# Kernel optimization log

Hardware: AMD Instinct MI355X
Metric: run time of the kernel (lower is better)

Reference implementation:

```python
import jax, jax.numpy as jnp
import numpy as np

C = 64; H = 80; W = 120; B = 2; V = 3; BV = B * V; D = 20
NEAR = 0.1; FAR = 100.0
BF16 = jnp.bfloat16


def conv2d(x, w, b, pad):
    y = jax.lax.conv_general_dilated(x, w, (1, 1), [(pad, pad), (pad, pad)],
                                     dimension_numbers=('NCHW', 'OIHW', 'NCHW'))
    return y + b[None, :, None, None]


def bn2d(x, g, b, m, v, eps=1e-5):
    # BatchNorm2d in inference mode (running stats)
    scale = g / jnp.sqrt(v + eps)
    return (x - m[None, :, None, None]) * scale[None, :, None, None] + b[None, :, None, None]


def grid_sample(feat, grid):
    # feat [N,C,Hf,Wf], grid [N,Hg,Wg,2] in [-1,1]; bilinear, zeros padding, align_corners=True
    _, _, Hf, Wf = feat.shape
    gx = (grid[..., 0] + 1.0) * 0.5 * (Wf - 1)
    gy = (grid[..., 1] + 1.0) * 0.5 * (Hf - 1)
    x0 = jnp.floor(gx); y0 = jnp.floor(gy)

    def one(f, gx, gy, x0, y0):
        def gather(xi, yi):
            valid = (xi >= 0) & (xi < Wf) & (yi >= 0) & (yi < Hf)
            xc = jnp.clip(xi, 0, Wf - 1).astype(jnp.int32)
            yc = jnp.clip(yi, 0, Hf - 1).astype(jnp.int32)
            return f[:, yc, xc] * valid.astype(f.dtype)
        wx = gx - x0; wy = gy - y0
        return (gather(x0, y0) * ((1 - wx) * (1 - wy))
                + gather(x0 + 1, y0) * (wx * (1 - wy))
                + gather(x0, y0 + 1) * ((1 - wx) * wy)
                + gather(x0 + 1, y0 + 1) * (wx * wy))
    return jax.vmap(one)(feat, gx, gy, x0, y0)


def forward(x, intrinsics, c2ws,
            pf_bn1_g, pf_bn1_b, pf_bn1_m, pf_bn1_v, pf_w1, pf_b1,
            pf_bn2_g, pf_bn2_b, pf_bn2_m, pf_bn2_v, pf_w2, pf_b2,
            cp_w, cp_b, cf_bn_g, cf_bn_b, cf_bn_m, cf_bn_v, cf_w, cf_b):
    # ---- flag[0]: predicted depth -> world xyz, position_fusion ----
    depth = 255.0 * (0.5 * jnp.tanh(x[:, 0]) + 0.5)                       # [BV,H,W]
    d16 = depth.astype(BF16)
    ug = jnp.broadcast_to(jnp.arange(W, dtype=jnp.float32)[None, :], (H, W)).astype(BF16)
    vg = jnp.broadcast_to(jnp.arange(H, dtype=jnp.float32)[:, None], (H, W)).astype(BF16)
    cam = jnp.stack([ug[None] * d16, vg[None] * d16, d16], axis=-1).reshape(BV, H * W, 3)
    Kinv = jnp.linalg.inv(intrinsics.astype(jnp.float32)).astype(BF16)
    xyz = jnp.einsum('nij,npj->npi', Kinv, cam)                           # cam coords
    xyz = jnp.einsum('nij,npj->npi', c2ws[:, :3, :3].astype(BF16), xyz) \
          + c2ws[:, :3, 3].astype(BF16)[:, None, :]                       # world coords
    xyz = xyz.reshape(BV, H, W, 3).transpose(0, 3, 1, 2).astype(x.dtype)
    h = jnp.concatenate([xyz, x], axis=1)                                 # [BV,C+3,H,W]
    h = jax.nn.silu(conv2d(bn2d(h, pf_bn1_g, pf_bn1_b, pf_bn1_m, pf_bn1_v), pf_w1, pf_b1, 4))
    h = jax.nn.silu(conv2d(bn2d(h, pf_bn2_g, pf_bn2_b, pf_bn2_m, pf_bn2_v), pf_w2, pf_b2, 4))

    # ---- flag[1]: multi-view plane-sweep correlation ----
    xr = h.reshape(B, V, C, H, W)
    vb = lambda t: t.transpose(1, 0, 2, 3, 4).reshape(BV, C, H, W)        # 'b v ... -> (v b) ...'
    feat01 = vb(xr)
    Ki = intrinsics.reshape(B, V, 3, 3)
    intr_curr = jax.lax.stop_gradient(
        (Ki * jnp.array([W, H, 1.0], jnp.float32)[None, None, :, None]).transpose(1, 0, 2, 3).reshape(BV, 3, 3))
    E = jax.lax.stop_gradient(c2ws.reshape(B, V, 4, 4))
    Einv = jnp.linalg.inv(E)
    dmin, dmax = 1.0 / FAR, 1.0 / NEAR
    depth_vals = 1.0 / (dmin + jnp.linspace(0.0, 1.0, D) * (dmax - dmin))  # [D]
    pix = jnp.stack([jnp.broadcast_to(jnp.arange(W, dtype=jnp.float32)[None, :], (H, W)),
                     jnp.broadcast_to(jnp.arange(H, dtype=jnp.float32)[:, None], (H, W)),
                     jnp.ones((H, W), jnp.float32)], 0).reshape(3, H * W)
    Kinv_c = jnp.linalg.inv(intr_curr).astype(BF16)

    corr = 0.0
    for idx in range(1, V):
        order = list(range(V))[idx:] + list(range(V))[:idx]
        feat10 = vb(xr[:, jnp.array(order)])                              # [BV,C,H,W]
        pose = jnp.concatenate([E[:, o] @ Einv[:, v0] for v0, o in enumerate(order)], axis=0)  # [BV,4,4]
        pts = jnp.einsum('bij,jp->bip', Kinv_c, pix.astype(BF16))
        pts = jnp.einsum('bij,bjp->bip', pose[:, :3, :3].astype(BF16), pts)
        pts = pts[:, :, None, :] * depth_vals.astype(BF16)[None, None, :, None] \
              + pose[:, :3, 3].astype(BF16)[:, :, None, None]             # [BV,3,D,HW]
        pts = jnp.einsum('bij,bjdp->bidp', intr_curr.astype(BF16), pts).astype(jnp.float32)
        den = jnp.maximum(pts[:, 2], 1e-3)
        grid = jnp.stack([2.0 * pts[:, 0] / den / (W - 1) - 1.0,
                          2.0 * pts[:, 1] / den / (H - 1) - 1.0], axis=-1)
        grid = jax.lax.stop_gradient(grid.reshape(BV, D * H, W, 2))
        warped = grid_sample(feat10, grid).reshape(BV, C, D, H, W)
        corr = corr + jnp.einsum('bchw,bcdhw->bdhw', feat01, warped) / (C ** 0.5)
    corr = corr / (V - 1)

    cin = jnp.concatenate([corr, feat01], axis=1)                         # [BV,D+C,H,W]
    cost = conv2d(cin, cp_w, cp_b, 1).reshape(V, B, C, H, W).transpose(1, 0, 2, 3, 4)
    fused = jnp.concatenate([cost, xr], axis=2).reshape(BV, 2 * C, H, W)
    out = jax.nn.silu(conv2d(bn2d(fused, cf_bn_g, cf_bn_b, cf_bn_m, cf_bn_v), cf_w, cf_b, 4))
    return out


def setup_inputs() -> dict:
    key = jax.random.key(0)
    ks = jax.random.split(key, 24)
    def nrm(i, shape, scale=1.0):
        return scale * jax.random.normal(ks[i], shape, jnp.float32)
    def wconv(i, shape):
        fan_in = int(np.prod(shape[1:]))
        return jax.random.normal(ks[i], shape, jnp.float32) / np.sqrt(fan_in)
    x = nrm(0, (BV, C, H, W))
    Kmat = np.tile(np.array([[1.2, 0, 0.5], [0, 1.6, 0.5], [0, 0, 1.0]], np.float32), (BV, 1, 1))
    intrinsics = jnp.asarray(Kmat)
    c2_list = []
    for i in range(BV):
        th = 0.3 * (i % V) - 0.3
        T = np.eye(4, dtype=np.float32)
        T[:3, :3] = np.array([[np.cos(th), 0, np.sin(th)], [0, 1, 0], [-np.sin(th), 0, np.cos(th)]], np.float32)
        T[:3, 3] = [0.5 * (i % V) - 0.5, 0.0, 0.1]
        c2_list.append(T)
    c2ws = jnp.asarray(np.stack(c2_list))
    # first BN sees raw world-xyz channels (magnitude ~1e4), so realistic running var there
    bn1_v = jnp.concatenate([jnp.full((3,), 1e8, jnp.float32), jnp.ones((C,), jnp.float32)])
    return dict(
        x=x, intrinsics=intrinsics, c2ws=c2ws,
        pf_bn1_g=1.0 + 0.1 * nrm(1, (C + 3,)), pf_bn1_b=0.1 * nrm(2, (C + 3,)),
        pf_bn1_m=0.1 * nrm(3, (C + 3,)), pf_bn1_v=bn1_v,
        pf_w1=wconv(4, (C, C + 3, 9, 9)), pf_b1=0.01 * nrm(5, (C,)),
        pf_bn2_g=1.0 + 0.1 * nrm(6, (C,)), pf_bn2_b=0.1 * nrm(7, (C,)),
        pf_bn2_m=0.1 * nrm(8, (C,)), pf_bn2_v=jnp.ones((C,), jnp.float32),
        pf_w2=wconv(9, (C, C, 9, 9)), pf_b2=0.01 * nrm(10, (C,)),
        cp_w=wconv(11, (C, C + D, 3, 3)), cp_b=0.01 * nrm(12, (C,)),
        cf_bn_g=1.0 + 0.1 * nrm(13, (2 * C,)), cf_bn_b=0.1 * nrm(14, (2 * C,)),
        cf_bn_m=0.1 * nrm(15, (2 * C,)), cf_bn_v=jnp.ones((2 * C,), jnp.float32),
        cf_w=wconv(16, (C, 2 * C, 9, 9)), cf_b=0.01 * nrm(17, (C,)))


def reference(x, intrinsics, c2ws,
              pf_bn1_g, pf_bn1_b, pf_bn1_m, pf_bn1_v, pf_w1, pf_b1,
              pf_bn2_g, pf_bn2_b, pf_bn2_m, pf_bn2_v, pf_w2, pf_b2,
              cp_w, cp_b, cf_bn_g, cf_bn_b, cf_bn_m, cf_bn_v, cf_w, cf_b):
    return forward(x, intrinsics, c2ws,
                   pf_bn1_g, pf_bn1_b, pf_bn1_m, pf_bn1_v, pf_w1, pf_b1,
                   pf_bn2_g, pf_bn2_b, pf_bn2_m, pf_bn2_v, pf_w2, pf_b2,
                   cp_w, cp_b, cf_bn_g, cf_bn_b, cf_bn_m, cf_bn_v, cf_w, cf_b)
```

## Files before the change

kernel.cpp:

```cpp
#include <hip/hip_runtime.h>
#include <math.h>

static constexpr int kH  = 80;
static constexpr int kW  = 120;
static constexpr int kHW = kH * kW;
static constexpr int kBV = 6;
static constexpr int kD  = 20;

typedef __attribute__((ext_vector_type(8)))  short bf16x8;
typedef __attribute__((ext_vector_type(16))) float f32x16;
typedef __attribute__((ext_vector_type(4)))  int   i32x4;
typedef __attribute__((ext_vector_type(2)))  int   i32x2;
typedef __attribute__((ext_vector_type(4)))  float float4v;

__device__ __forceinline__ float bf16r(float x) {
  unsigned u = __float_as_uint(x);
  u += 0x7FFFu + ((u >> 16) & 1u);
  return __uint_as_float(u & 0xFFFF0000u);
}
__device__ __forceinline__ unsigned short bf16c(float x) {
  unsigned u = __float_as_uint(x);
  u += 0x7FFFu + ((u >> 16) & 1u);
  return (unsigned short)(u >> 16);
}
__device__ __forceinline__ int pack2(float a, float b) {
  return (int)((unsigned)bf16c(a) | ((unsigned)bf16c(b) << 16));
}
__device__ __forceinline__ float bl(unsigned pk) {
  return __uint_as_float(pk << 16);
}
__device__ __forceinline__ float bh(unsigned pk) {
  return __uint_as_float(pk & 0xFFFF0000u);
}

struct ConstBuf {
  float bn1_s[67], bn1_o[67];
  float bn2_s[64], bn2_o[64];
  float bnf_s[128], bnf_o[128];
  float Kinv[6][9];
  float Rw[6][9];
  float tw[6][3];
  float Kinvc[6][9];
  float intrc[6][9];
  float poseR[2][6][9];
  float poseT[2][6][3];
  float dvals[20];
};

__device__ void inv3x3(const float* A, float* o) {
  float a = A[0], b = A[1], c = A[2];
  float d = A[3], e = A[4], f = A[5];
  float g = A[6], h = A[7], i = A[8];
  float det = a * (e * i - f * h) - b * (d * i - f * g) + c * (d * h - e * g);
  float id = 1.0f / det;
  o[0] = (e * i - f * h) * id;
  o[1] = -(b * i - c * h) * id;
  o[2] = (b * f - c * e) * id;
  o[3] = -(d * i - f * g) * id;
  o[4] = (a * i - c * g) * id;
  o[5] = -(a * f - c * d) * id;
  o[6] = (d * h - e * g) * id;
  o[7] = -(a * h - b * g) * id;
  o[8] = (a * e - b * d) * id;
}

__device__ void inv4x4(const float* A, float* out) {
  float M[4][8];
  for (int r = 0; r < 4; ++r) {
    for (int c = 0; c < 4; ++c) M[r][c] = A[r * 4 + c];
    for (int c = 0; c < 4; ++c) M[r][4 + c] = (r == c) ? 1.0f : 0.0f;
  }
  for (int col = 0; col < 4; ++col) {
    int p = col;
    float best = fabsf(M[col][col]);
    for (int r = col + 1; r < 4; ++r) {
      float v = fabsf(M[r][col]);
      if (v > best) { best = v; p = r; }
    }
    if (p != col)
      for (int c = 0; c < 8; ++c) { float t = M[col][c]; M[col][c] = M[p][c]; M[p][c] = t; }
    float inv = 1.0f / M[col][col];
    for (int c = 0; c < 8; ++c) M[col][c] *= inv;
    for (int r = 0; r < 4; ++r) {
      if (r == col) continue;
      float f = M[r][col];
      for (int c = 0; c < 8; ++c) M[r][c] -= f * M[col][c];
    }
  }
  for (int r = 0; r < 4; ++r)
    for (int c = 0; c < 4; ++c) out[r * 4 + c] = M[r][4 + c];
}

__device__ void mm4(const float* A, const float* B, float* C) {
  for (int r = 0; r < 4; ++r)
    for (int c = 0; c < 4; ++c) {
      float s = 0.0f;
      for (int k = 0; k < 4; ++k) s += A[r * 4 + k] * B[k * 4 + c];
      C[r * 4 + c] = s;
    }
}

__global__ void consts_kernel(const float* __restrict__ intr, const float* __restrict__ c2,
                              const float* g1, const float* b1, const float* m1, const float* v1,
                              const float* g2, const float* b2, const float* m2, const float* v2,
                              const float* gf, const float* bff, const float* mf, const float* vff,
                              ConstBuf* cb) {
  int tid = threadIdx.x;
  for (int c = tid; c < 67; c += 64) {
    float s = g1[c] / sqrtf(v1[c] + 1e-5f);
    cb->bn1_s[c] = s; cb->bn1_o[c] = b1[c] - m1[c] * s;
  }
  for (int c = tid; c < 64; c += 64) {
    float s = g2[c] / sqrtf(v2[c] + 1e-5f);
    cb->bn2_s[c] = s; cb->bn2_o[c] = b2[c] - m2[c] * s;
  }
  for (int c = tid; c < 128; c += 64) {
    float s = gf[c] / sqrtf(vff[c] + 1e-5f);
    cb->bnf_s[c] = s; cb->bnf_o[c] = bff[c] - mf[c] * s;
  }
  if (tid < 20) {
    float l = (1.0f / 19.0f) * (float)tid;
    cb->dvals[tid] = bf16r(1.0f / (0.01f + l * 9.99f));
  }
  __shared__ float Einv_s[6][16];
  if (tid < 6) {
    float Ki[9];
    inv3x3(intr + tid * 9, Ki);
    for (int k = 0; k < 9; ++k) cb->Kinv[tid][k] = bf16r(Ki[k]);
    const float* T = c2 + tid * 16;
    cb->Rw[tid][0] = bf16r(T[0]);  cb->Rw[tid][1] = bf16r(T[1]);  cb->Rw[tid][2] = bf16r(T[2]);
    cb->Rw[tid][3] = bf16r(T[4]);  cb->Rw[tid][4] = bf16r(T[5]);  cb->Rw[tid][5] = bf16r(T[6]);
    cb->Rw[tid][6] = bf16r(T[8]);  cb->Rw[tid][7] = bf16r(T[9]);  cb->Rw[tid][8] = bf16r(T[10]);
    cb->tw[tid][0] = bf16r(T[3]);  cb->tw[tid][1] = bf16r(T[7]);  cb->tw[tid][2] = bf16r(T[11]);
    inv4x4(T, Einv_s[tid]);
    int vj = tid >> 1, bj = tid & 1, ii = bj * 3 + vj;
    const float* Kk = intr + ii * 9;
    float S[9] = {Kk[0] * 120.0f, Kk[1] * 120.0f, Kk[2] * 120.0f,
                  Kk[3] * 80.0f,  Kk[4] * 80.0f,  Kk[5] * 80.0f,
                  Kk[6],          Kk[7],          Kk[8]};
    for (int k = 0; k < 9; ++k) cb->intrc[tid][k] = bf16r(S[k]);
    float Si[9];
    inv3x3(S, Si);
    for (int k = 0; k < 9; ++k) cb->Kinvc[tid][k] = bf16r(Si[k]);
  }
  __syncthreads();
  if (tid < 12) {
    int t = tid / 6, jj = tid % 6;
    int vj = jj >> 1, bj = jj & 1;
    int o = (vj + t + 1) % 3;
    float P[16];
    mm4(c2 + (bj * 3 + o) * 16, Einv_s[bj * 3 + vj], P);
    for (int r = 0; r < 3; ++r) {
      for (int c = 0; c < 3; ++c) cb->poseR[t][jj][r * 3 + c] = bf16r(P[r * 4 + c]);
      cb->poseT[t][jj][r] = bf16r(P[r * 4 + 3]);
    }
  }
}

template <int K, int CINP, int CINR>
__global__ __launch_bounds__(256)
void prep_w(const float* __restrict__ w, unsigned short* __restrict__ Wp) {
  constexpr int NCH = CINP / 32;
  constexpr int NU = K * K * NCH * 256;
  int u = blockIdx.x * 256 + threadIdx.x;
  if (u >= NU) return;
  int slot = u & 255;
  int rest = u >> 8;
  int ci = rest % NCH;
  int kk = rest / NCH;
  int ky = kk / K, kx = kk - ky * K;
  int q = slot >> 6, lu = slot & 63;
  int nt = q >> 1, kc = q & 1;
  int oc = nt * 32 + (lu & 31);
  int gi = kc * 2 + (lu >> 5);
  int chb = ci * 32 + gi * 8;
  unsigned short o[8];
#pragma unroll
  for (int e = 0; e < 8; ++e) {
    int ch = chb + e;
    float val = (ch < CINR) ? w[(((size_t)oc * CINR + ch) * K + ky) * K + kx] : 0.0f;
    o[e] = bf16c(val);
  }
  i32x4 pk;
  pk.x = (int)o[0] | ((int)o[1] << 16);
  pk.y = (int)o[2] | ((int)o[3] << 16);
  pk.z = (int)o[4] | ((int)o[5] << 16);
  pk.w = (int)o[6] | ((int)o[7] << 16);
  *(i32x4*)&Wp[(size_t)u * 8] = pk;
}

__global__ __launch_bounds__(256)
void hn_pack(const float* __restrict__ x, const ConstBuf* __restrict__ cb,
             unsigned short* __restrict__ hn_b) {
  int id = blockIdx.x * 256 + threadIdx.x;
  if (id >= kBV * kHW) return;
  int bv = id / kHW, pix = id - bv * kHW;
  int yy = pix / kW, xx = pix - yy * kW;
  float t0 = tanhf(x[(size_t)bv * 64 * kHW + pix]);
  float depth = 255.0f * (0.5f * t0 + 0.5f);
  float dz = bf16r(depth);
  float cx = bf16r((float)xx * dz);
  float cy = bf16r((float)yy * dz);
  const float* Ki = cb->Kinv[bv];
  float p0 = bf16r(Ki[0] * cx + Ki[1] * cy + Ki[2] * dz);
  float p1 = bf16r(Ki[3] * cx + Ki[4] * cy + Ki[5] * dz);
  float p2 = bf16r(Ki[6] * cx + Ki[7] * cy + Ki[8] * dz);
  const float* R = cb->Rw[bv];
  const float* tw = cb->tw[bv];
  float q[3];
  q[0] = bf16r(bf16r(R[0] * p0 + R[1] * p1 + R[2] * p2) + tw[0]);
  q[1] = bf16r(bf16r(R[3] * p0 + R[4] * p1 + R[5] * p2) + tw[1]);
  q[2] = bf16r(bf16r(R[6] * p0 + R[7] * p1 + R[8] * p2) + tw[2]);
  unsigned short* o = &hn_b[(size_t)id * 96];
  const float* xb = x + (size_t)bv * 64 * kHW + pix;
#pragma unroll
  for (int g = 0; g < 24; ++g) {
    float vv[4];
#pragma unroll
    for (int e = 0; e < 4; ++e) {
      int ch = g * 4 + e;
      float val;
      if (ch < 3) val = q[ch] * cb->bn1_s[ch] + cb->bn1_o[ch];
      else if (ch < 67) val = xb[(size_t)(ch - 3) * kHW] * cb->bn1_s[ch] + cb->bn1_o[ch];
      else val = 0.0f;
      vv[e] = val;
    }
    i32x2 pk = {pack2(vv[0], vv[1]), pack2(vv[2], vv[3])};
    *(i32x2*)(o + g * 4) = pk;
  }
}

template <int CINP, int K, int OUT>
__global__ __launch_bounds__(256)
void conv_mfma(const unsigned short* __restrict__ in_b,
               const unsigned short* __restrict__ Wp,
               const float* __restrict__ bias,
               const ConstBuf* __restrict__ cb,
               float* __restrict__ outf,
               unsigned short* __restrict__ outb,
               unsigned short* __restrict__ outb2) {
  constexpr int NCH = CINP / 32;
  constexpr int KK = K * K;
  constexpr int KH0 = (KK + 1) / 2;
  constexpr int PAD = K / 2;
  constexpr int NC = 16 + K - 1;
  constexpr int NR = 8 + K - 1;
  constexpr int NPX = NC * NR;
  __shared__ unsigned short sA[NPX * 32];

  const int tid = threadIdx.x;
  const int w = tid >> 6, l = tid & 63;
  const int half = w >> 1, mp = w & 1;
  const int bx = blockIdx.x, by = blockIdx.y, bz = blockIdx.z;
  const size_t inbase = (size_t)bz * kHW;

  const int r = l & 31, h = l >> 5;
  const int xloc = r & 15, rhi = r >> 4;
  const int kk0 = half ? KH0 : 0;
  const int myKK = half ? (KK - KH0) : KH0;
  f32x16 acc[2][2] = {};

  for (int ci = 0; ci < NCH; ++ci) {
    __syncthreads();
    for (int g2 = tid; g2 < NPX * 4; g2 += 256) {
      int px = g2 >> 2, gi = g2 & 3;
      int hy = px / NC, hx = px - hy * NC;
      int gy = by * 8 - PAD + hy, gx = bx * 16 - PAD + hx;
      bool ok = ((unsigned)gy < (unsigned)kH) && ((unsigned)gx < (unsigned)kW);
      i32x4 v = {0, 0, 0, 0};
      if (ok) v = *(const i32x4*)&in_b[(inbase + gy * kW + gx) * CINP + ci * 32 + gi * 8];
      *(i32x4*)&sA[px * 32 + ((gi ^ ((px >> 2) & 3)) << 3)] = v;
    }
    __syncthreads();

    const unsigned short* wb = Wp + ((size_t)ci * 256 + (size_t)kk0 * NCH * 256) * 8;
    const size_t kstep = (size_t)NCH * 256 * 8;
#define LOADB(dst, rdidx)                                                       \
    {                                                                           \
      const unsigned short* bp = wb + (size_t)(rdidx) * kstep + (size_t)l * 8;  \
      dst[0][0] = *(const bf16x8*)(bp);                                         \
      dst[0][1] = *(const bf16x8*)(bp + 64 * 8);                                \
      dst[1][0] = *(const bf16x8*)(bp + 128 * 8);                               \
      dst[1][1] = *(const bf16x8*)(bp + 192 * 8);                               \
    }
#define COMPUTE(rdidx, bb)                                                      \
    {                                                                           \
      const int kk = kk0 + (rdidx);                                             \
      const int ky = kk / K, kx = kk - ky * K;                                  \
      bf16x8 a[2][2];                                                           \
      _Pragma("unroll")                                                         \
      for (int m = 0; m < 2; ++m) {                                             \
        const int hp = (4 * mp + 2 * m + rhi + ky) * NC + (xloc + kx);          \
        _Pragma("unroll")                                                       \
        for (int kc = 0; kc < 2; ++kc) {                                        \
          int gi = kc * 2 + h;                                                  \
          a[m][kc] = *(const bf16x8*)&sA[hp * 32 + ((gi ^ ((hp >> 2) & 3)) << 3)]; \
        }                                                                       \
      }                                                                         \
      _Pragma("unroll")                                                         \
      for (int m = 0; m < 2; ++m)                                               \
        _Pragma("unroll")                                                       \
        for (int nt = 0; nt < 2; ++nt) {                                        \
          acc[m][nt] = __builtin_amdgcn_mfma_f32_32x32x16_bf16(a[m][0], bb[nt][0], acc[m][nt], 0, 0, 0); \
          acc[m][nt] = __builtin_amdgcn_mfma_f32_32x32x16_bf16(a[m][1], bb[nt][1], acc[m][nt], 0, 0, 0); \
        }                                                                       \
    }

    bf16x8 b0[2][2], b1[2][2];
    LOADB(b0, 0);
    int rd = 0;
    for (; rd + 2 <= myKK; rd += 2) {
      LOADB(b1, rd + 1);
      COMPUTE(rd, b0);
      if (rd + 2 < myKK) LOADB(b0, rd + 2);
      COMPUTE(rd + 1, b1);
    }
    if (rd < myKK) COMPUTE(rd, b0);
#undef LOADB
#undef COMPUTE
  }

  float* scratch = (float*)sA;
#pragma unroll
  for (int cm = 0; cm < 2; ++cm) {
#pragma unroll
    for (int cn = 0; cn < 2; ++cn) {
      float* sp = scratch + ((mp * 64 + l) * 16);
      __syncthreads();
      if (half == 1) {
#pragma unroll
        for (int q = 0; q < 16; ++q) sp[q] = acc[cm][cn][q];
      }
      __syncthreads();
      if (half == 0) {
#pragma unroll
        for (int q = 0; q < 16; ++q) acc[cm][cn][q] += sp[q];
      }
    }
  }
  if (half == 1) return;

#pragma unroll
  for (int m = 0; m < 2; ++m) {
#pragma unroll
    for (int nt = 0; nt < 2; ++nt) {
      const int oc = nt * 32 + (l & 31);
      const float bs = bias[oc];
      float s2 = 0.f, o2 = 0.f;
      if (OUT == 0) { s2 = cb->bn2_s[oc]; o2 = cb->bn2_o[oc]; }
      if (OUT == 1) { s2 = cb->bnf_s[64 + oc]; o2 = cb->bnf_o[64 + oc]; }
      if (OUT == 2) { s2 = cb->bnf_s[oc]; o2 = cb->bnf_o[oc]; }
#pragma unroll
      for (int reg = 0; reg < 16; ++reg) {
        int row = (reg & 3) + 8 * (reg >> 2) + 4 * h;
        int x = bx * 16 + (row & 15);
        if (x >= kW) continue;
        int y = by * 8 + 4 * mp + 2 * m + (row >> 4);
        float v = acc[m][nt][reg] + bs;
        if (OUT != 2) v = v / (1.0f + expf(-v));
        if (OUT == 0) {
          size_t px = inbase + y * kW + x;
          outb[px * 64 + oc] = bf16c(v * s2 + o2);
        } else if (OUT == 1) {
          size_t px = inbase + y * kW + x;
          outb[px * 64 + oc] = bf16c(v);
          outb2[px * 128 + 64 + oc] = bf16c(v * s2 + o2);
        } else if (OUT == 2) {
          int i = (bz & 1) * 3 + (bz >> 1);
          size_t px = (size_t)i * kHW + y * kW + x;
          outb[px * 128 + oc] = bf16c(v * s2 + o2);
        } else {
          outf[((size_t)bz * 64 + oc) * kHW + y * kW + x] = v;
        }
      }
    }
  }
}

__global__ __launch_bounds__(256)
void corr_kernel(const unsigned short* __restrict__ h_b, const ConstBuf* __restrict__ cb,
                 unsigned short* __restrict__ cin_b) {
  __shared__ float sgeo[4][2][40][8];
  const int tid = threadIdx.x;
  const int w = tid >> 6, lane = tid & 63;
  const int pair = blockIdx.x * 4 + w;
  const int j = pair / (kHW / 2);
  const int pix = (pair - j * (kHW / 2)) * 2;
  const int b = j & 1, v = j >> 1;
  const int ph = lane >> 5, cl = lane & 31;
  const int pixl = pix + ph;
  const int dst = b * 3 + v;
  const unsigned f01pk =
      ((const unsigned*)(h_b + ((size_t)dst * kHW + pixl) * 64))[cl];
  const float f01lo = bl(f01pk), f01hi = bh(f01pk);
  const char* sb0 = (const char*)(h_b + (size_t)(b * 3 + ((v + 1) % 3)) * kHW * 64);
  const char* sb1 = (const char*)(h_b + (size_t)(b * 3 + ((v + 2) % 3)) * kHW * 64);

  for (int job = lane; job < 80; job += 64) {
    const int p = job / 40, jj = job - p * 40;
    const int d = jj >> 1, t = jj & 1;
    const int pp = pix + p;
    const int yyp = pp / kW, xxp = pp - yyp * kW;
    const float* Kc = cb->Kinvc[j];
    const float* IC = cb->intrc[j];
    const float uf = (float)xxp, vf = (float)yyp;
    float p1_0 = bf16r(Kc[0] * uf + Kc[1] * vf + Kc[2]);
    float p1_1 = bf16r(Kc[3] * uf + Kc[4] * vf + Kc[5]);
    float p1_2 = bf16r(Kc[6] * uf + Kc[7] * vf + Kc[8]);
    const float* PR = cb->poseR[t][j];
    const float* PT = cb->poseT[t][j];
    float p20 = bf16r(PR[0] * p1_0 + PR[1] * p1_1 + PR[2] * p1_2);
    float p21 = bf16r(PR[3] * p1_0 + PR[4] * p1_1 + PR[5] * p1_2);
    float p22 = bf16r(PR[6] * p1_0 + PR[7] * p1_1 + PR[8] * p1_2);
    float dv = cb->dvals[d];
    float q0 = bf16r(bf16r(p20 * dv) + PT[0]);
    float q1 = bf16r(bf16r(p21 * dv) + PT[1]);
    float q2 = bf16r(bf16r(p22 * dv) + PT[2]);
    float s0 = bf16r(IC[0] * q0 + IC[1] * q1 + IC[2] * q2);
    float s1 = bf16r(IC[3] * q0 + IC[4] * q1 + IC[5] * q2);
    float s2 = bf16r(IC[6] * q0 + IC[7] * q1 + IC[8] * q2);
    float den = fmaxf(s2, 1e-3f);
    float g0 = 2.0f * s0 / den / 119.0f - 1.0f;
    float g1 = 2.0f * s1 / den / 79.0f - 1.0f;
    float gx = (g0 + 1.0f) * 0.5f * 119.0f;
    float gy = (g1 + 1.0f) * 0.5f * 79.0f;
    float x0f = floorf(gx), y0f = floorf(gy);
    float wx = gx - x0f, wy = gy - y0f;
    float x1f = x0f + 1.0f, y1f = y0f + 1.0f;
    float vx0 = (x0f >= 0.0f && x0f < 120.0f) ? 1.0f : 0.0f;
    float vx1 = (x1f >= 0.0f && x1f < 120.0f) ? 1.0f : 0.0f;
    float vy0 = (y0f >= 0.0f && y0f < 80.0f) ? 1.0f : 0.0f;
    float vy1 = (y1f >= 0.0f && y1f < 80.0f) ? 1.0f : 0.0f;
    int xi0 = (int)fminf(fmaxf(x0f, 0.0f), 119.0f);
    int xi1 = (int)fminf(fmaxf(x1f, 0.0f), 119.0f);
    int yi0 = (int)fminf(fmaxf(y0f, 0.0f), 79.0f);
    int yi1 = (int)fminf(fmaxf(y1f, 0.0f), 79.0f);
    int r0b = yi0 * (kW * 128), r1b = yi1 * (kW * 128);
    int c0b = xi0 * 128, c1b = xi1 * 128;
    float* gp = sgeo[w][p][jj];
    gp[0] = __int_as_float(r0b + c0b);
    gp[1] = __int_as_float(r0b + c1b);
    gp[2] = __int_as_float(r1b + c0b);
    gp[3] = __int_as_float(r1b + c1b);
    gp[4] = ((1.0f - wx) * (1.0f - wy)) * (vx0 * vy0);
    gp[5] = (wx * (1.0f - wy)) * (vx1 * vy0);
    gp[6] = ((1.0f - wx) * wy) * (vx0 * vy1);
    gp[7] = (wx * wy) * (vx1 * vy1);
  }
  __syncthreads();

  unsigned short* op = &cin_b[(size_t)(j * kHW + pixl) * 96];
  *(unsigned*)(op + 20 + 2 * cl) = f01pk;
  if (cl < 6) *(unsigned*)(op + 84 + 2 * cl) = 0u;

  const unsigned cl4 = (unsigned)cl * 4u;
#pragma unroll 2
  for (int d = 0; d < kD; ++d) {
    float a = 0.0f;
#pragma unroll
    for (int t = 0; t < 2; ++t) {
      const char* sb = t ? sb1 : sb0;
      const float* gp = sgeo[w][ph][d * 2 + t];
      float4v ga = *(const float4v*)gp;
      float4v gb = *(const float4v*)(gp + 4);
      unsigned k00 = *(const unsigned*)(sb + ((unsigned)__float_as_int(ga.x) + cl4));
      unsigned k10 = *(const unsigned*)(sb + ((unsigned)__float_as_int(ga.y) + cl4));
      unsigned k01 = *(const unsigned*)(sb + ((unsigned)__float_as_int(ga.z) + cl4));
      unsigned k11 = *(const unsigned*)(sb + ((unsigned)__float_as_int(ga.w) + cl4));
      float al = gb.x * bl(k00) + gb.y * bl(k10) + gb.z * bl(k01) + gb.w * bl(k11);
      float ah = gb.x * bh(k00) + gb.y * bh(k10) + gb.z * bh(k01) + gb.w * bh(k11);
      a += al * f01lo + ah * f01hi;
    }
#pragma unroll
    for (int off = 16; off > 0; off >>= 1) a += __shfl_xor(a, off, 64);
    if (cl == 0) op[d] = bf16c(a * 0.0625f);
  }
}

extern "C" void kernel_launch(void* const* d_in, const int* in_sizes, int n_in,
                              void* d_out, int out_size, void* d_ws, size_t ws_size,
                              hipStream_t stream) {
  (void)in_sizes; (void)n_in; (void)out_size; (void)ws_size;
  const float* x    = (const float*)d_in[0];
  const float* intr = (const float*)d_in[1];
  const float* c2w  = (const float*)d_in[2];
  const float* bn1g = (const float*)d_in[3];
  const float* bn1b = (const float*)d_in[4];
  const float* bn1m = (const float*)d_in[5];
  const float* bn1v = (const float*)d_in[6];
  const float* w1   = (const float*)d_in[7];
  const float* b1   = (const float*)d_in[8];
  const float* bn2g = (const float*)d_in[9];
  const float* bn2b = (const float*)d_in[10];
  const float* bn2m = (const float*)d_in[11];
  const float* bn2v = (const float*)d_in[12];
  const float* w2   = (const float*)d_in[13];
  const float* b2   = (const float*)d_in[14];
  const float* cpw  = (const float*)d_in[15];
  const float* cpb  = (const float*)d_in[16];
  const float* bnfg = (const float*)d_in[17];
  const float* bnfb = (const float*)d_in[18];
  const float* bnfm = (const float*)d_in[19];
  const float* bnfv = (const float*)d_in[20];
  const float* wf   = (const float*)d_in[21];
  const float* bff  = (const float*)d_in[22];

  char* ws = (char*)d_ws;
  ConstBuf* cb            = (ConstBuf*)ws;
  unsigned short* hn_b    = (unsigned short*)(ws + 8192);
  unsigned short* h1_b    = (unsigned short*)(ws + 11067392);
  unsigned short* h_b     = (unsigned short*)(ws + 18440192);
  unsigned short* cin_b   = (unsigned short*)(ws + 33185792);
  unsigned short* fused_b = (unsigned short*)(ws + 44244992);
  unsigned short* Wp1     = (unsigned short*)(ws + 58990592);
  unsigned short* Wp2     = (unsigned short*)(ws + 59985920);
  unsigned short* Wpc     = (unsigned short*)(ws + 60649472);
  unsigned short* Wpf     = (unsigned short*)(ws + 60760064);

  consts_kernel<<<1, 64, 0, stream>>>(intr, c2w, bn1g, bn1b, bn1m, bn1v,
                                      bn2g, bn2b, bn2m, bn2v, bnfg, bnfb, bnfm, bnfv, cb);
  prep_w<9, 96, 67><<<243, 256, 0, stream>>>(w1, Wp1);
  prep_w<9, 64, 64><<<162, 256, 0, stream>>>(w2, Wp2);
  prep_w<3, 96, 84><<<27, 256, 0, stream>>>(cpw, Wpc);
  prep_w<9, 128, 128><<<324, 256, 0, stream>>>(wf, Wpf);
  hn_pack<<<225, 256, 0, stream>>>(x, cb, hn_b);

  dim3 cgrid(8, 10, 6);
  conv_mfma<96, 9, 0><<<cgrid, 256, 0, stream>>>(hn_b, Wp1, b1, cb, nullptr, h1_b, nullptr);
  conv_mfma<64, 9, 1><<<cgrid, 256, 0, stream>>>(h1_b, Wp2, b2, cb, nullptr, h_b, fused_b);
  corr_kernel<<<7200, 256, 0, stream>>>(h_b, cb, cin_b);
  conv_mfma<96, 3, 2><<<cgrid, 256, 0, stream>>>(cin_b, Wpc, cpb, cb, nullptr, fused_b, nullptr);
  conv_mfma<128, 9, 3><<<cgrid, 256, 0, stream>>>(fused_b, Wpf, bff, cb, (float*)d_out, nullptr, nullptr);
}
```

Before: 339.3 us.

## Reuse A fragments across kx via DPP lane shift instead of LDS reloads

Within each kernel row, the A operand for kx>0 is the previous fragment shifted by one lane. A DPP row_shr-style update now produces it, and only the boundary lane (xloc==15) reloads from LDS. The split between the two wave halves is realigned to whole kernel rows so every half starts at kx=0. This cuts LDS read traffic per MFMA. In exchange the pipeline now has divergent patch loads, runtime ping-pong buffer selection with a pointer, and DPP latency, which may add register pressure or scheduling stalls.

```diff
diff --git a/kernel.cpp b/kernel.cpp
--- a/kernel.cpp
+++ b/kernel.cpp
@@ -230,6 +230,16 @@
   }
 }
 
+#define SHIFTF(v)                                                              \
+  {                                                                            \
+    i32x4 _u = *(i32x4*)&(v);                                                  \
+    _u.x = __builtin_amdgcn_update_dpp(_u.x, _u.x, 0x101, 0xF, 0xF, false);    \
+    _u.y = __builtin_amdgcn_update_dpp(_u.y, _u.y, 0x101, 0xF, 0xF, false);    \
+    _u.z = __builtin_amdgcn_update_dpp(_u.z, _u.z, 0x101, 0xF, 0xF, false);    \
+    _u.w = __builtin_amdgcn_update_dpp(_u.w, _u.w, 0x101, 0xF, 0xF, false);    \
+    *(i32x4*)&(v) = _u;                                                        \
+  }
+
 template <int CINP, int K, int OUT>
 __global__ __launch_bounds__(256)
 void conv_mfma(const unsigned short* __restrict__ in_b,
@@ -241,7 +251,8 @@
                unsigned short* __restrict__ outb2) {
   constexpr int NCH = CINP / 32;
   constexpr int KK = K * K;
-  constexpr int KH0 = (KK + 1) / 2;
+  constexpr int KROW0 = (K == 9) ? 5 : 2;
+  constexpr int KH0 = KROW0 * K;
   constexpr int PAD = K / 2;
   constexpr int NC = 16 + K - 1;
   constexpr int NR = 8 + K - 1;
@@ -258,6 +269,7 @@
   const int xloc = r & 15, rhi = r >> 4;
   const int kk0 = half ? KH0 : 0;
   const int myKK = half ? (KK - KH0) : KH0;
+  const bool patchlane = (xloc == 15);
   f32x16 acc[2][2] = {};
 
   for (int ci = 0; ci < NCH; ++ci) {
@@ -283,41 +295,50 @@
       dst[1][0] = *(const bf16x8*)(bp + 128 * 8);                               \
       dst[1][1] = *(const bf16x8*)(bp + 192 * 8);                               \
     }
-#define COMPUTE(rdidx, bb)                                                      \
-    {                                                                           \
-      const int kk = kk0 + (rdidx);                                             \
-      const int ky = kk / K, kx = kk - ky * K;                                  \
-      bf16x8 a[2][2];                                                           \
-      _Pragma("unroll")                                                         \
-      for (int m = 0; m < 2; ++m) {                                             \
-        const int hp = (4 * mp + 2 * m + rhi + ky) * NC + (xloc + kx);          \
-        _Pragma("unroll")                                                       \
-        for (int kc = 0; kc < 2; ++kc) {                                        \
-          int gi = kc * 2 + h;                                                  \
-          a[m][kc] = *(const bf16x8*)&sA[hp * 32 + ((gi ^ ((hp >> 2) & 3)) << 3)]; \
-        }                                                                       \
-      }                                                                         \
-      _Pragma("unroll")                                                         \
-      for (int m = 0; m < 2; ++m)                                               \
-        _Pragma("unroll")                                                       \
-        for (int nt = 0; nt < 2; ++nt) {                                        \
-          acc[m][nt] = __builtin_amdgcn_mfma_f32_32x32x16_bf16(a[m][0], bb[nt][0], acc[m][nt], 0, 0, 0); \
-          acc[m][nt] = __builtin_amdgcn_mfma_f32_32x32x16_bf16(a[m][1], bb[nt][1], acc[m][nt], 0, 0, 0); \
-        }                                                                       \
-    }
 
     bf16x8 b0[2][2], b1[2][2];
+    bf16x8 a[2][2];
     LOADB(b0, 0);
-    int rd = 0;
-    for (; rd + 2 <= myKK; rd += 2) {
-      LOADB(b1, rd + 1);
-      COMPUTE(rd, b0);
-      if (rd + 2 < myKK) LOADB(b0, rd + 2);
-      COMPUTE(rd + 1, b1);
-    }
-    if (rd < myKK) COMPUTE(rd, b0);
+    int kx = 0, ky = kk0 / K;
+    for (int rd = 0; rd < myKK; ++rd) {
+      if (rd + 1 < myKK) {
+        if (rd & 1) { LOADB(b0, rd + 1); } else { LOADB(b1, rd + 1); }
+      }
+      if (kx == 0) {
+#pragma unroll
+        for (int m = 0; m < 2; ++m) {
+          const int hp = (4 * mp + 2 * m + rhi + ky) * NC + xloc;
+#pragma unroll
+          for (int kc = 0; kc < 2; ++kc) {
+            int gi = kc * 2 + h;
+            a[m][kc] = *(const bf16x8*)&sA[hp * 32 + ((gi ^ ((hp >> 2) & 3)) << 3)];
+          }
+        }
+      } else {
+        SHIFTF(a[0][0]); SHIFTF(a[0][1]); SHIFTF(a[1][0]); SHIFTF(a[1][1]);
+        if (patchlane) {
+#pragma unroll
+          for (int m = 0; m < 2; ++m) {
+            const int hp = (4 * mp + 2 * m + rhi + ky) * NC + (15 + kx);
+#pragma unroll
+            for (int kc = 0; kc < 2; ++kc) {
+              int gi = kc * 2 + h;
+              a[m][kc] = *(const bf16x8*)&sA[hp * 32 + ((gi ^ ((hp >> 2) & 3)) << 3)];
+            }
+          }
+        }
+      }
+      bf16x8 (*bb)[2] = (rd & 1) ? b1 : b0;
+#pragma unroll
+      for (int m = 0; m < 2; ++m)
+#pragma unroll
+        for (int nt = 0; nt < 2; ++nt) {
+          acc[m][nt] = __builtin_amdgcn_mfma_f32_32x32x16_bf16(a[m][0], bb[nt][0], acc[m][nt], 0, 0, 0);
+          acc[m][nt] = __builtin_amdgcn_mfma_f32_32x32x16_bf16(a[m][1], bb[nt][1], acc[m][nt], 0, 0, 0);
+        }
+      if (++kx == K) { kx = 0; ++ky; }
+    }
 #undef LOADB
-#undef COMPUTE
   }
 
   float* scratch = (float*)sA;
```

New measurement: 426.0 us. 1.26x slower.
